# Kernel tuning notes

Hardware: AMD Instinct MI355X
Metric: run time of the kernel (lower is better)

The kernel has to match this reference:

```python
import jax, jax.numpy as jnp
import numpy as np

B, N, F = 512, 64, 64
ROBOT_DIM, HUMAN_DIM, HID = 9, 5, 128
K = 3  # Chebyshev order


def setup_inputs() -> dict:
    key = jax.random.key(0)
    ks = jax.random.split(key, 16)
    # complete directed graph without self loops, shared across the batch
    src, dst = np.nonzero(~np.eye(N, dtype=bool))
    edge_index = jnp.asarray(np.stack([src, dst]), dtype=jnp.int32)  # [2, E]
    s = 0.05
    return {
        "robot_x": jax.random.normal(ks[0], (B, 1, ROBOT_DIM), jnp.float32),
        "human_x": jax.random.normal(ks[1], (B, N - 1, HUMAN_DIM), jnp.float32),
        "edge_index": edge_index,
        "wr1_w": jax.random.normal(ks[2], (ROBOT_DIM, HID), jnp.float32) * s,
        "wr1_b": jax.random.normal(ks[3], (HID,), jnp.float32) * s,
        "wr2_w": jax.random.normal(ks[4], (HID, F), jnp.float32) * s,
        "wr2_b": jax.random.normal(ks[5], (F,), jnp.float32) * s,
        "wh1_w": jax.random.normal(ks[6], (HUMAN_DIM, HID), jnp.float32) * s,
        "wh1_b": jax.random.normal(ks[7], (HID,), jnp.float32) * s,
        "wh2_w": jax.random.normal(ks[8], (HID, F), jnp.float32) * s,
        "wh2_b": jax.random.normal(ks[9], (F,), jnp.float32) * s,
        "cheb_w": jax.random.normal(ks[10], (K, F, F), jnp.float32) * s,
        "cheb_b": jax.random.normal(ks[11], (F,), jnp.float32) * s,
    }


def reference(robot_x, human_x, edge_index, wr1_w, wr1_b, wr2_w, wr2_b,
              wh1_w, wh1_b, wh2_w, wh2_b, cheb_w, cheb_b):
    # MLP embeddings with last_relu=True
    r = jax.nn.relu(robot_x @ wr1_w + wr1_b)
    r = jax.nn.relu(r @ wr2_w + wr2_b)            # [B, 1, F]
    h = jax.nn.relu(human_x @ wh1_w + wh1_b)
    h = jax.nn.relu(h @ wh2_w + wh2_b)            # [B, N-1, F]
    X = jnp.concatenate([r, h], axis=1)           # [B, N, F]

    src, dst = edge_index[0], edge_index[1]
    n = X.shape[1]
    # PyG ChebConv sym-normalized scaled Laplacian with lambda_max=2:
    # L_hat = -D^{-1/2} A D^{-1/2}  (edge weights all ones, no self loops)
    deg = jax.ops.segment_sum(jnp.ones(src.shape[0], X.dtype), src, num_segments=n)
    dinv = jnp.where(deg > 0, deg ** -0.5, 0.0)
    w = -(dinv[src] * dinv[dst])                  # [E]

    def prop(x):  # x: [B, N, F] -> L_hat @ x per batch via gather/scatter
        msg = x[:, src, :] * w[None, :, None]     # [B, E, F]
        return jnp.zeros_like(x).at[:, dst, :].add(msg)

    Tx0 = X
    Tx1 = prop(X)
    Tx2 = 2.0 * prop(Tx1) - Tx0
    Tx = jnp.stack([Tx0, Tx1, Tx2], axis=0)       # [K, B, N, F]
    out = jnp.einsum("kbnf,kfo->bno", Tx, cheb_w) + cheb_b
    return out[:, 0, :]                           # robot node output [B, F]
```

## Files before the change

kernel.cpp:

```cpp
#include <hip/hip_runtime.h>


#define BDIM 256

typedef __attribute__((ext_vector_type(8))) short bf16x8;
typedef __attribute__((ext_vector_type(4))) float f32x4;
typedef __attribute__((ext_vector_type(4))) unsigned int u32x4;

static __device__ __forceinline__ unsigned int cvt_pk_bf16(float lo, float hi) {
    unsigned int r;
    asm("v_cvt_pk_bf16_f32 %0, %1, %2" : "=v"(r) : "v"(lo), "v"(hi));
    return r;
}

__global__ __launch_bounds__(256, 2) void dgcrnn_mfma(
    const float* __restrict__ robot_x,
    const float* __restrict__ human_x,
    const float* __restrict__ wr1, const float* __restrict__ wr1_b,
    const float* __restrict__ wr2, const float* __restrict__ wr2_b,
    const float* __restrict__ wh1, const float* __restrict__ wh1_b,
    const float* __restrict__ wh2, const float* __restrict__ wh2_b,
    const float* __restrict__ cw,  const float* __restrict__ cb,
    float* __restrict__ out)
{
    __shared__ float x_lds[324];
    __shared__ float wh2b_l[64], wr2b_l[64], cb_l[64];
    __shared__ float rrow[128];
    __shared__ __align__(16) unsigned int wh2T[4096];
    __shared__ __align__(16) short fragA[8192];
    __shared__ __align__(16) float rp_red[256];
    __shared__ float hpart[256];

    const int t    = threadIdx.x;
    const int b    = blockIdx.x;
    const int l    = t & 63;
    const int w    = t >> 6;
    const int o0   = (t & 15) * 4;
    const int fgrp = t >> 4;

    f32x4 wr2q[8];
    #pragma unroll
    for (int j = 0; j < 8; ++j)
        wr2q[j] = *(const f32x4*)&wr2[(fgrp * 8 + j) * 64 + o0];

    const int k0 = ((t >> 6) & 3) * 32 + ((t >> 4) & 3) * 8;
    f32x4 wv4[10], bias4[2];
    #pragma unroll
    for (int i = 0; i < 5; ++i) {
        wv4[2 * i]     = *(const f32x4*)&wh1[i * 128 + k0];
        wv4[2 * i + 1] = *(const f32x4*)&wh1[i * 128 + k0 + 4];
    }
    bias4[0] = *(const f32x4*)&wh1_b[k0];
    bias4[1] = *(const f32x4*)&wh1_b[k0 + 4];

    float wr1c[9], wr1bb = 0.f;
    if (t < 128) {
        #pragma unroll
        for (int i = 0; i < 9; ++i) wr1c[i] = wr1[i * 128 + t];
        wr1bb = wr1_b[t];
    }

    for (int i = t; i < 324; i += BDIM)
        x_lds[i] = (i < 9) ? robot_x[b * 9 + i] : human_x[b * 315 + (i - 9)];
    if (t < 64) { wh2b_l[t] = wh2_b[t]; wr2b_l[t] = wr2_b[t]; cb_l[t] = cb[t]; }
    {
        f32x4 e[4], d[4];
        #pragma unroll
        for (int kk = 0; kk < 4; ++kk) {
            int kp = fgrp * 4 + kk;
            e[kk] = *(const f32x4*)&wh2[(2 * kp) * 64 + o0];
            d[kk] = *(const f32x4*)&wh2[(2 * kp + 1) * 64 + o0];
        }
        #pragma unroll
        for (int c = 0; c < 4; ++c) {
            int o = o0 + c;
            u32x4 vv;
            #pragma unroll
            for (int kk = 0; kk < 4; ++kk) vv[kk] = cvt_pk_bf16(e[kk][c], d[kk][c]);
            *(u32x4*)&wh2T[o * 64 + ((fgrp * 4) ^ ((o & 15) << 2))] = vv;
        }
    }
    __syncthreads();

    #pragma unroll
    for (int s = 0; s < 4; ++s) {
        int slot = s * 256 + t;
        int row  = (s << 4) | (t & 15);
        u32x4 vv = {0u, 0u, 0u, 0u};
        if (row != 63) {
            float a8[8];
            #pragma unroll
            for (int j = 0; j < 8; ++j) a8[j] = bias4[j >> 2][j & 3];
            #pragma unroll
            for (int i = 0; i < 5; ++i) {
                float xv = x_lds[9 + row * 5 + i];
                #pragma unroll
                for (int j = 0; j < 8; ++j)
                    a8[j] = fmaf(xv, wv4[2 * i + (j >> 2)][j & 3], a8[j]);
            }
            #pragma unroll
            for (int jw = 0; jw < 4; ++jw)
                vv[jw] = cvt_pk_bf16(fmaxf(a8[2 * jw], 0.f), fmaxf(a8[2 * jw + 1], 0.f));
        }
        *(u32x4*)&fragA[slot * 8] = vv;
    }
    if (t < 128) {
        float a = wr1bb;
        #pragma unroll
        for (int i = 0; i < 9; ++i) a = fmaf(x_lds[i], wr1c[i], a);
        rrow[t] = fmaxf(a, 0.f);
    }
    __syncthreads();

    {
        const int c = l & 15, g = l >> 4, mt = w;
        bf16x8 af[4];
        #pragma unroll
        for (int kt = 0; kt < 4; ++kt)
            af[kt] = *reinterpret_cast<const bf16x8*>(&fragA[((mt * 4 + kt) * 64 + l) * 8]);
        #pragma unroll
        for (int nt = 0; nt < 4; ++nt) {
            const int o = nt * 16 + c;
            f32x4 acc = {0.f, 0.f, 0.f, 0.f};
            #pragma unroll
            for (int kt = 0; kt < 4; ++kt) {
                int kw0 = kt * 16 + g * 4;
                bf16x8 bfv = *reinterpret_cast<const bf16x8*>(
                    &wh2T[o * 64 + (kw0 ^ (c << 2))]);
                acc = __builtin_amdgcn_mfma_f32_16x16x32_bf16(af[kt], bfv, acc, 0, 0, 0);
            }
            float bias = wh2b_l[o];
            float s4 = 0.f;
            #pragma unroll
            for (int reg = 0; reg < 4; ++reg) {
                int node = mt * 16 + g * 4 + reg;
                float hv = fmaxf(acc[reg] + bias, 0.f);
                s4 += (node == 63) ? 0.f : hv;
            }
            s4 += __shfl_xor(s4, 16, 64);
            s4 += __shfl_xor(s4, 32, 64);
            if (g == 0) hpart[mt * 64 + o] = s4;
        }
    }

    f32x4 cwq[4][3];
    #pragma unroll
    for (int ff = 0; ff < 4; ++ff)
        #pragma unroll
        for (int k = 0; k < 3; ++k)
            cwq[ff][k] = *(const f32x4*)&cw[k * 4096 + (fgrp * 4 + ff) * 64 + o0];

    {
        f32x4 rp = {0.f, 0.f, 0.f, 0.f};
        #pragma unroll
        for (int j = 0; j < 8; ++j) {
            float hv = rrow[fgrp * 8 + j];
            #pragma unroll
            for (int c = 0; c < 4; ++c) rp[c] = fmaf(hv, wr2q[j][c], rp[c]);
        }
        #pragma unroll
        for (int c = 0; c < 4; ++c) {
            float v = rp[c];
            v += __shfl_xor(v, 16, 64);
            v += __shfl_xor(v, 32, 64);
            rp[c] = v;
        }
        if (l < 16) *(f32x4*)&rp_red[w * 64 + o0] = rp;
    }
    __syncthreads();

    {
        const float c1 = 1.0f / 63.0f;
        const float c2 = 2.0f / 3969.0f - 1.0f;
        const float c3 = 124.0f / 3969.0f;
        f32x4 a4 = {0.f, 0.f, 0.f, 0.f};
        #pragma unroll
        for (int ff = 0; ff < 4; ++ff) {
            int f = fgrp * 4 + ff;
            float rsum = wr2b_l[f] + rp_red[f] + rp_red[64 + f]
                       + rp_red[128 + f] + rp_red[192 + f];
            float rv = fmaxf(rsum, 0.f);
            float sv = rv + hpart[f] + hpart[64 + f] + hpart[128 + f] + hpart[192 + f];
            #pragma unroll
            for (int c = 0; c < 4; ++c) {
                float w0  = cwq[ff][0][c];
                float w1  = cwq[ff][1][c];
                float w2v = cwq[ff][2][c];
                a4[c] += rv * (w0 + c1 * w1 + c2 * w2v) + sv * (c3 * w2v - c1 * w1);
            }
        }
        #pragma unroll
        for (int c = 0; c < 4; ++c) {
            float v = a4[c];
            v += __shfl_xor(v, 16, 64);
            v += __shfl_xor(v, 32, 64);
            a4[c] = v;
        }
        float* out_part = reinterpret_cast<float*>(fragA);
        if (l < 16) *(f32x4*)&out_part[w * 64 + o0] = a4;
    }
    __syncthreads();

    if (t < 64) {
        const float* out_part = reinterpret_cast<const float*>(fragA);
        out[b * 64 + t] = cb_l[t] + out_part[t] + out_part[64 + t]
                        + out_part[128 + t] + out_part[192 + t];
    }
}

extern "C" void kernel_launch(void* const* d_in, const int* in_sizes, int n_in,
                              void* d_out, int out_size, void* d_ws, size_t ws_size,
                              hipStream_t stream) {
    const float* robot_x = (const float*)d_in[0];
    const float* human_x = (const float*)d_in[1];
    const float* wr1   = (const float*)d_in[3];
    const float* wr1_b = (const float*)d_in[4];
    const float* wr2   = (const float*)d_in[5];
    const float* wr2_b = (const float*)d_in[6];
    const float* wh1   = (const float*)d_in[7];
    const float* wh1_b = (const float*)d_in[8];
    const float* wh2   = (const float*)d_in[9];
    const float* wh2_b = (const float*)d_in[10];
    const float* cw    = (const float*)d_in[11];
    const float* cb    = (const float*)d_in[12];
    float* out = (float*)d_out;

    dgcrnn_mfma<<<512, BDIM, 0, stream>>>(robot_x, human_x,
                                          wr1, wr1_b, wr2, wr2_b,
                                          wh1, wh1_b, wh2, wh2_b,
                                          cw, cb, out);
}
```

Baseline: 11.44 us.

## Process two batch items per 512-thread block sharing the transposed wh2 tile

Each block now runs 512 threads and handles two batch elements, one per half, with per-half LDS buffers. The bf16 transposed wh2 tile is built once and shared, and each half writes only half of it. The launch grid drops from 512 blocks to 256. The cheb weight loads are hoisted earlier so their latency overlaps the setup phase. This is meant to halve the per-block weight staging cost, but it leaves only 256 blocks on the device and raises register and LDS pressure per block.

```diff
diff --git a/kernel.cpp b/kernel.cpp
--- a/kernel.cpp
+++ b/kernel.cpp
@@ -1,11 +1,12 @@
 #include <hip/hip_runtime.h>
 
 
-#define BDIM 256
+#define BDIM 512
 
 typedef __attribute__((ext_vector_type(8))) short bf16x8;
 typedef __attribute__((ext_vector_type(4))) float f32x4;
 typedef __attribute__((ext_vector_type(4))) unsigned int u32x4;
+typedef __attribute__((ext_vector_type(2))) unsigned int u32x2;
 
 static __device__ __forceinline__ unsigned int cvt_pk_bf16(float lo, float hi) {
     unsigned int r;
@@ -13,7 +14,7 @@
     return r;
 }
 
-__global__ __launch_bounds__(256, 2) void dgcrnn_mfma(
+__global__ __launch_bounds__(512, 2) void dgcrnn_mfma(
     const float* __restrict__ robot_x,
     const float* __restrict__ human_x,
     const float* __restrict__ wr1, const float* __restrict__ wr1_b,
@@ -23,27 +24,29 @@
     const float* __restrict__ cw,  const float* __restrict__ cb,
     float* __restrict__ out)
 {
-    __shared__ float x_lds[324];
+    __shared__ float x_lds[2][324];
     __shared__ float wh2b_l[64], wr2b_l[64], cb_l[64];
-    __shared__ float rrow[128];
+    __shared__ float rrow[2][128];
     __shared__ __align__(16) unsigned int wh2T[4096];
-    __shared__ __align__(16) short fragA[8192];
-    __shared__ __align__(16) float rp_red[256];
-    __shared__ float hpart[256];
+    __shared__ __align__(16) short fragA[2][8192];
+    __shared__ __align__(16) float rp_red[2][256];
+    __shared__ float hpart[2][256];
 
     const int t    = threadIdx.x;
-    const int b    = blockIdx.x;
-    const int l    = t & 63;
-    const int w    = t >> 6;
-    const int o0   = (t & 15) * 4;
-    const int fgrp = t >> 4;
+    const int half = t >> 8;
+    const int tt   = t & 255;
+    const int b2   = blockIdx.x * 2 + half;
+    const int l    = tt & 63;
+    const int wh_  = (t >> 6) & 3;
+    const int o0   = (tt & 15) * 4;
+    const int fgrp = tt >> 4;
 
     f32x4 wr2q[8];
     #pragma unroll
     for (int j = 0; j < 8; ++j)
         wr2q[j] = *(const f32x4*)&wr2[(fgrp * 8 + j) * 64 + o0];
 
-    const int k0 = ((t >> 6) & 3) * 32 + ((t >> 4) & 3) * 8;
+    const int k0 = ((tt >> 6) & 3) * 32 + ((tt >> 4) & 3) * 8;
     f32x4 wv4[10], bias4[2];
     #pragma unroll
     for (int i = 0; i < 5; ++i) {
@@ -54,38 +57,45 @@
     bias4[1] = *(const f32x4*)&wh1_b[k0 + 4];
 
     float wr1c[9], wr1bb = 0.f;
-    if (t < 128) {
-        #pragma unroll
-        for (int i = 0; i < 9; ++i) wr1c[i] = wr1[i * 128 + t];
-        wr1bb = wr1_b[t];
-    }
-
-    for (int i = t; i < 324; i += BDIM)
-        x_lds[i] = (i < 9) ? robot_x[b * 9 + i] : human_x[b * 315 + (i - 9)];
+    if (tt < 128) {
+        #pragma unroll
+        for (int i = 0; i < 9; ++i) wr1c[i] = wr1[i * 128 + tt];
+        wr1bb = wr1_b[tt];
+    }
+
+    f32x4 cwq[4][3];
+    #pragma unroll
+    for (int ff = 0; ff < 4; ++ff)
+        #pragma unroll
+        for (int k = 0; k < 3; ++k)
+            cwq[ff][k] = *(const f32x4*)&cw[k * 4096 + (fgrp * 4 + ff) * 64 + o0];
+
+    for (int i = tt; i < 324; i += 256)
+        x_lds[half][i] = (i < 9) ? robot_x[b2 * 9 + i] : human_x[b2 * 315 + (i - 9)];
     if (t < 64) { wh2b_l[t] = wh2_b[t]; wr2b_l[t] = wr2_b[t]; cb_l[t] = cb[t]; }
     {
-        f32x4 e[4], d[4];
-        #pragma unroll
-        for (int kk = 0; kk < 4; ++kk) {
-            int kp = fgrp * 4 + kk;
+        f32x4 e[2], d[2];
+        #pragma unroll
+        for (int kk = 0; kk < 2; ++kk) {
+            int kp = fgrp * 4 + 2 * half + kk;
             e[kk] = *(const f32x4*)&wh2[(2 * kp) * 64 + o0];
             d[kk] = *(const f32x4*)&wh2[(2 * kp + 1) * 64 + o0];
         }
         #pragma unroll
         for (int c = 0; c < 4; ++c) {
             int o = o0 + c;
-            u32x4 vv;
-            #pragma unroll
-            for (int kk = 0; kk < 4; ++kk) vv[kk] = cvt_pk_bf16(e[kk][c], d[kk][c]);
-            *(u32x4*)&wh2T[o * 64 + ((fgrp * 4) ^ ((o & 15) << 2))] = vv;
+            u32x2 vv;
+            #pragma unroll
+            for (int kk = 0; kk < 2; ++kk) vv[kk] = cvt_pk_bf16(e[kk][c], d[kk][c]);
+            *(u32x2*)&wh2T[o * 64 + ((fgrp * 4) ^ ((o & 15) << 2)) + 2 * half] = vv;
         }
     }
     __syncthreads();
 
     #pragma unroll
     for (int s = 0; s < 4; ++s) {
-        int slot = s * 256 + t;
-        int row  = (s << 4) | (t & 15);
+        int slot = s * 256 + tt;
+        int row  = (s << 4) | (tt & 15);
         u32x4 vv = {0u, 0u, 0u, 0u};
         if (row != 63) {
             float a8[8];
@@ -93,7 +103,7 @@
             for (int j = 0; j < 8; ++j) a8[j] = bias4[j >> 2][j & 3];
             #pragma unroll
             for (int i = 0; i < 5; ++i) {
-                float xv = x_lds[9 + row * 5 + i];
+                float xv = x_lds[half][9 + row * 5 + i];
                 #pragma unroll
                 for (int j = 0; j < 8; ++j)
                     a8[j] = fmaf(xv, wv4[2 * i + (j >> 2)][j & 3], a8[j]);
@@ -102,22 +112,23 @@
             for (int jw = 0; jw < 4; ++jw)
                 vv[jw] = cvt_pk_bf16(fmaxf(a8[2 * jw], 0.f), fmaxf(a8[2 * jw + 1], 0.f));
         }
-        *(u32x4*)&fragA[slot * 8] = vv;
-    }
-    if (t < 128) {
+        *(u32x4*)&fragA[half][slot * 8] = vv;
+    }
+    if (tt < 128) {
         float a = wr1bb;
         #pragma unroll
-        for (int i = 0; i < 9; ++i) a = fmaf(x_lds[i], wr1c[i], a);
-        rrow[t] = fmaxf(a, 0.f);
-    }
-    __syncthreads();
-
-    {
-        const int c = l & 15, g = l >> 4, mt = w;
+        for (int i = 0; i < 9; ++i) a = fmaf(x_lds[half][i], wr1c[i], a);
+        rrow[half][tt] = fmaxf(a, 0.f);
+    }
+    __syncthreads();
+
+    {
+        const int c = l & 15, g = l >> 4, mt = wh_;
         bf16x8 af[4];
         #pragma unroll
         for (int kt = 0; kt < 4; ++kt)
-            af[kt] = *reinterpret_cast<const bf16x8*>(&fragA[((mt * 4 + kt) * 64 + l) * 8]);
+            af[kt] = *reinterpret_cast<const bf16x8*>(
+                &fragA[half][((mt * 4 + kt) * 64 + l) * 8]);
         #pragma unroll
         for (int nt = 0; nt < 4; ++nt) {
             const int o = nt * 16 + c;
@@ -139,22 +150,15 @@
             }
             s4 += __shfl_xor(s4, 16, 64);
             s4 += __shfl_xor(s4, 32, 64);
-            if (g == 0) hpart[mt * 64 + o] = s4;
-        }
-    }
-
-    f32x4 cwq[4][3];
-    #pragma unroll
-    for (int ff = 0; ff < 4; ++ff)
-        #pragma unroll
-        for (int k = 0; k < 3; ++k)
-            cwq[ff][k] = *(const f32x4*)&cw[k * 4096 + (fgrp * 4 + ff) * 64 + o0];
+            if (g == 0) hpart[half][mt * 64 + o] = s4;
+        }
+    }
 
     {
         f32x4 rp = {0.f, 0.f, 0.f, 0.f};
         #pragma unroll
         for (int j = 0; j < 8; ++j) {
-            float hv = rrow[fgrp * 8 + j];
+            float hv = rrow[half][fgrp * 8 + j];
             #pragma unroll
             for (int c = 0; c < 4; ++c) rp[c] = fmaf(hv, wr2q[j][c], rp[c]);
         }
@@ -165,7 +169,7 @@
             v += __shfl_xor(v, 32, 64);
             rp[c] = v;
         }
-        if (l < 16) *(f32x4*)&rp_red[w * 64 + o0] = rp;
+        if (l < 16) *(f32x4*)&rp_red[half][wh_ * 64 + o0] = rp;
     }
     __syncthreads();
 
@@ -177,10 +181,11 @@
         #pragma unroll
         for (int ff = 0; ff < 4; ++ff) {
             int f = fgrp * 4 + ff;
-            float rsum = wr2b_l[f] + rp_red[f] + rp_red[64 + f]
-                       + rp_red[128 + f] + rp_red[192 + f];
+            float rsum = wr2b_l[f] + rp_red[half][f] + rp_red[half][64 + f]
+                       + rp_red[half][128 + f] + rp_red[half][192 + f];
             float rv = fmaxf(rsum, 0.f);
-            float sv = rv + hpart[f] + hpart[64 + f] + hpart[128 + f] + hpart[192 + f];
+            float sv = rv + hpart[half][f] + hpart[half][64 + f]
+                     + hpart[half][128 + f] + hpart[half][192 + f];
             #pragma unroll
             for (int c = 0; c < 4; ++c) {
                 float w0  = cwq[ff][0][c];
@@ -196,15 +201,15 @@
             v += __shfl_xor(v, 32, 64);
             a4[c] = v;
         }
-        float* out_part = reinterpret_cast<float*>(fragA);
-        if (l < 16) *(f32x4*)&out_part[w * 64 + o0] = a4;
-    }
-    __syncthreads();
-
-    if (t < 64) {
-        const float* out_part = reinterpret_cast<const float*>(fragA);
-        out[b * 64 + t] = cb_l[t] + out_part[t] + out_part[64 + t]
-                        + out_part[128 + t] + out_part[192 + t];
+        float* out_part = reinterpret_cast<float*>(fragA[half]);
+        if (l < 16) *(f32x4*)&out_part[wh_ * 64 + o0] = a4;
+    }
+    __syncthreads();
+
+    if (tt < 64) {
+        const float* out_part = reinterpret_cast<const float*>(fragA[half]);
+        out[b2 * 64 + tt] = cb_l[tt] + out_part[tt] + out_part[64 + tt]
+                          + out_part[128 + tt] + out_part[192 + tt];
     }
 }
 
@@ -225,7 +230,7 @@
     const float* cb    = (const float*)d_in[12];
     float* out = (float*)d_out;
 
-    dgcrnn_mfma<<<512, BDIM, 0, stream>>>(robot_x, human_x,
+    dgcrnn_mfma<<<256, BDIM, 0, stream>>>(robot_x, human_x,
                                           wr1, wr1_b, wr2, wr2_b,
                                           wh1, wh1_b, wh2, wh2_b,
                                           cw, cb, out);
```

Result: slower. 11.86 us (+3.7%).
